# Kernel tuning notes

Hardware: AMD Instinct MI355X
Metric: run time of the kernel (lower is better)

The kernel has to match this reference:

```python
import jax, jax.numpy as jnp
import numpy as np

BATCH, DIM = 32, 512
STDDEV = 0.1


def _annihilation(dim):
    # diag(sqrt(1..dim-1), k=1), complex64
    d = jnp.sqrt(jnp.arange(1, dim, dtype=jnp.float32)).astype(jnp.complex64)
    return jnp.diag(d, k=1)


def setup_inputs() -> dict:
    key = jax.random.key(0)
    ks = jax.random.split(key, 8)
    f = lambda k, shape: jax.random.normal(k, shape, dtype=jnp.float32)
    return {
        'inputs_re': f(ks[0], (BATCH, DIM, DIM)),
        'inputs_im': f(ks[1], (BATCH, DIM, DIM)),
        'theta_1': f(ks[2], (1,)) * STDDEV,
        'theta_2': f(ks[3], (1,)) * STDDEV,
        'r': f(ks[4], (1,)) * STDDEV,
        'bx': f(ks[5], (1,)) * STDDEV,
        'bp': f(ks[6], (1,)) * STDDEV,
        'kappa': f(ks[7], (1,)) * STDDEV,
    }


def _forward(inputs_re, inputs_im, theta_1, theta_2, r, bx, bp, kappa):
    dim = inputs_re.shape[-1]
    x = jax.lax.complex(inputs_re, inputs_im)  # [B, dim, dim] complex64

    a = _annihilation(dim)                     # [dim, dim]
    a_dag = a.conj().T
    n_diag = jnp.arange(dim, dtype=jnp.float32).astype(jnp.complex64)  # number-operator diagonal

    # Rotation operators: expm(-1i*theta*N) with N diagonal -> closed-form diagonal exp (same math)
    th1 = theta_1[0].astype(jnp.complex64)
    th2 = theta_2[0].astype(jnp.complex64)
    R1 = jnp.diag(jnp.exp(-1j * th1 * n_diag))
    R2 = jnp.diag(jnp.exp(-1j * th2 * n_diag))

    # Kerr operator: expm(1i*kappa * (N*N elementwise)) ; N diagonal so N*N = diag(k^2)
    kap = kappa[0].astype(jnp.complex64)
    K = jnp.diag(jnp.exp(1j * kap * n_diag * n_diag))

    # Squeezing: in the TF source, '*' is ELEMENTWISE, and adjoint(a) (subdiag) elementwise
    # times a (superdiag) is the zero matrix -> generator is identically 0 -> S = expm(0) = I.
    # We keep the (zero) generator in the graph so r stays a (zero-grad) primal.
    r_c = r[0].astype(jnp.complex64)
    M_S = 0.5 * (r_c * (a_dag * a) - jnp.conj(r_c) * (a * a_dag))  # exactly zeros
    S = jnp.eye(dim, dtype=jnp.complex64) + M_S

    # Displacement: D = expm(alpha*a_dag - conj(alpha)*a). Generator M is skew-Hermitian,
    # so M = iH with H = -iM Hermitian; D = V diag(exp(i*w)) V^H via eigh (exact, differentiable).
    alpha = jax.lax.complex(bx[0], bp[0])
    M = alpha * a_dag - jnp.conj(alpha) * a
    H = (-1j) * M
    w, V = jnp.linalg.eigh(H)  # w real [dim], V [dim, dim]
    D = (V * jnp.exp(1j * w.astype(jnp.complex64))[None, :]) @ V.conj().T

    # Apply gates in the original order; operators are per-sample identical so
    # broadcast one [dim,dim] matrix over the batch instead of tiling.
    y = jnp.einsum('ij,bjk->bik', R1, x)
    y = jnp.einsum('ij,bjk->bik', S, y)
    y = jnp.einsum('ij,bjk->bik', R2, y)
    y = jnp.einsum('ij,bjk->bik', D, y)
    y = jnp.einsum('ij,bjk->bik', K, y)
    return y


def reference(inputs_re, inputs_im, theta_1, theta_2, r, bx, bp, kappa):
    return _forward(inputs_re, inputs_im, theta_1, theta_2, r, bx, bp, kappa)
```

## Files before the change

kernel.cpp:

```cpp
#include <hip/hip_runtime.h>
#include <hip/hip_fp16.h>

#define DIM 512
#define BATCH 32

typedef _Float16 half8 __attribute__((ext_vector_type(8)));
typedef float floatx4 __attribute__((ext_vector_type(4)));

static __device__ __forceinline__ unsigned short f2h(float f) {
    __half h = __float2half(f);
    return *reinterpret_cast<unsigned short*>(&h);
}

__global__ __launch_bounds__(256) void taylor_tables(const float* __restrict__ bxp,
                                                     const float* __restrict__ bpp,
                                                     const float* __restrict__ th1p,
                                                     const float* __restrict__ th2p,
                                                     const float* __restrict__ kapp,
                                                     float2* __restrict__ E,
                                                     float2* __restrict__ pm,
                                                     float2* __restrict__ pj) {
    if (blockIdx.x == 128) {
        for (int u = threadIdx.x; u < 2 * DIM; u += 256) {
            if (u < DIM) {
                float s, c;
                sincosf(kapp[0] * (float)(u * u), &s, &c);
                pm[u] = make_float2(c, s);
            } else {
                const int j = u - DIM;
                float s, c;
                sincosf(-(th1p[0] + th2p[0]) * (float)j, &s, &c);
                pj[j] = make_float2(c, s);
            }
        }
        return;
    }

    const int wave = (blockIdx.x * blockDim.x + threadIdx.x) >> 6;
    const int lane = threadIdx.x & 63;
    if (wave >= DIM) return;
    const int i = wave;
    const float bx = bxp[0], bp = bpp[0];
    const float invs = 0.5f;
    const int o = lane - 31;
    const int j = i + o;
    const bool jvalid = (j >= 0 && j < DIM);

    float pre = 0.f, pim = 0.f;
    if (o == -1 && i >= 1)      { float g = sqrtf((float)i)       * invs; pre =  bx * g; pim = bp * g; }
    if (o ==  1 && i + 1 < DIM) { float g = sqrtf((float)(i + 1)) * invs; pre = -bx * g; pim = bp * g; }
    float ere = (o == 0 ? 1.f : 0.f) + pre;
    float eim = pim;

    const float gs = (jvalid && j >= 1)       ? sqrtf((float)j)       * invs : 0.f;
    const float hs = (jvalid && j + 1 < DIM)  ? sqrtf((float)(j + 1)) * invs : 0.f;
    const float csup_re = -bx * gs, csup_im = bp * gs;
    const float csub_re =  bx * hs, csub_im = bp * hs;

    for (int k = 2; k <= 30; ++k) {
        const float invk = 1.f / (float)k;
        float pmre = __shfl_up(pre, 1, 64),   pmim = __shfl_up(pim, 1, 64);
        float ppre = __shfl_down(pre, 1, 64), ppim = __shfl_down(pim, 1, 64);
        if (lane == 0)  { pmre = 0.f; pmim = 0.f; }
        if (lane == 63) { ppre = 0.f; ppim = 0.f; }
        float nre = pmre * csup_re - pmim * csup_im + ppre * csub_re - ppim * csub_im;
        float nim = pmre * csup_im + pmim * csup_re + ppre * csub_im + ppim * csub_re;
        pre = nre * invk; pim = nim * invk;
        ere += pre; eim += pim;
    }

    for (int base = 0; base < DIM; base += 64) {
        const int c = base + lane;
        const int src = c - i + 31;
        const float tre = __shfl(ere, src & 63, 64);
        const float tim = __shfl(eim, src & 63, 64);
        float vre = 0.f, vim = 0.f;
        if (src >= 0 && src < 64) { vre = tre; vim = tim; }
        E[i * DIM + c] = make_float2(vre, vim);
    }
}

__global__ __launch_bounds__(256) void csq_fold32(const float2* __restrict__ A,
                                                  unsigned short* __restrict__ Gp,
                                                  const float2* __restrict__ pm,
                                                  const float2* __restrict__ pj) {
    __shared__ float2 At[16][33];
    __shared__ float2 Bt[16][33];
    const int j0 = blockIdx.x * 32, i0 = blockIdx.y * 32;
    const int tid = threadIdx.x;
    const int tx = tid & 15, ty = tid >> 4;
    const int lmin = max(0, max(i0, j0) - 32);
    const int lmax = min(DIM, min(i0, j0) + 64);

    float cre[2][2] = {{0.f}}, cim[2][2] = {{0.f}};
    for (int lt = lmin; lt < lmax; lt += 16) {
        for (int idx = tid; idx < 512; idx += 256) {
            const int r = idx >> 4, c = idx & 15;
            const int l = lt + c;
            At[c][r] = (l < lmax) ? A[(i0 + r) * DIM + l]       : make_float2(0.f, 0.f);
            Bt[c][r] = (l < lmax) ? A[(size_t)l * DIM + j0 + r] : make_float2(0.f, 0.f);
        }
        __syncthreads();
#pragma unroll
        for (int ll = 0; ll < 16; ++ll) {
            float2 a0 = At[ll][ty * 2], a1 = At[ll][ty * 2 + 1];
            float2 b0 = Bt[ll][tx * 2], b1 = Bt[ll][tx * 2 + 1];
            cre[0][0] += a0.x * b0.x - a0.y * b0.y;  cim[0][0] += a0.x * b0.y + a0.y * b0.x;
            cre[0][1] += a0.x * b1.x - a0.y * b1.y;  cim[0][1] += a0.x * b1.y + a0.y * b1.x;
            cre[1][0] += a1.x * b0.x - a1.y * b0.y;  cim[1][0] += a1.x * b0.y + a1.y * b0.x;
            cre[1][1] += a1.x * b1.x - a1.y * b1.y;  cim[1][1] += a1.x * b1.y + a1.y * b1.x;
        }
        __syncthreads();
    }

#pragma unroll
    for (int q = 0; q < 2; ++q) {
        const int m = i0 + ty * 2 + q;
        const float2 km = pm[m];
#pragma unroll
        for (int r = 0; r < 2; ++r) {
            const int j = j0 + tx * 2 + r;
            const float2 tj = pj[j];
            const float r1 = cre[q][r] * tj.x - cim[q][r] * tj.y;
            const float i1 = cre[q][r] * tj.y + cim[q][r] * tj.x;
            const float r2 = r1 * km.x - i1 * km.y;
            const float i2 = r1 * km.y + i1 * km.x;
            *reinterpret_cast<ushort2*>(Gp + (size_t)m * 1024 + 2 * j) =
                make_ushort2(f2h(r2), f2h(-i2));
        }
    }
}

#define XS_STRIDE 72
__global__ __launch_bounds__(256) void apply_fused(const unsigned short* __restrict__ Gp,
                                                   const float* __restrict__ xre,
                                                   const float* __restrict__ xim,
                                                   float* __restrict__ out) {
    __shared__ unsigned short Xs[128 * XS_STRIDE];

    const int k0 = blockIdx.x * 128, m0 = blockIdx.y * 128, b = blockIdx.z;
    const int tid = threadIdx.x, lane = tid & 63, w = tid >> 6;
    const int wr = w >> 1, wc = w & 1;
    const int lr = lane & 15, lk8 = (lane >> 4) * 8;

    const int jmin = max(0, m0 - 64);
    const int jmax = min(DIM, m0 + 192);
    const int nchunk = (jmax - jmin) >> 5;

    const int s_jl = tid & 31;
    const int s_k  = (tid >> 5) << 4;

    const unsigned short* gp = Gp + (size_t)(m0 + wr * 64 + lr) * 1024 + 2 * jmin + lk8;
    const unsigned short* bbase = &Xs[(wc * 64 + lr) * XS_STRIDE + lk8];

    floatx4 acc[4][4];
#pragma unroll
    for (int ms = 0; ms < 4; ++ms)
#pragma unroll
        for (int ns = 0; ns < 4; ++ns) {
            acc[ms][ns][0] = 0.f; acc[ms][ns][1] = 0.f;
            acc[ms][ns][2] = 0.f; acc[ms][ns][3] = 0.f;
        }

    for (int ch = 0; ch < nchunk; ++ch) {
        const size_t xrow = ((size_t)b * DIM + jmin + ch * 32 + s_jl) * DIM + k0 + s_k;
        float4 xr[4], xi[4];
#pragma unroll
        for (int t = 0; t < 4; ++t) xr[t] = *reinterpret_cast<const float4*>(xre + xrow + 4 * t);
#pragma unroll
        for (int t = 0; t < 4; ++t) xi[t] = *reinterpret_cast<const float4*>(xim + xrow + 4 * t);

        __syncthreads();

#pragma unroll
        for (int t = 0; t < 4; ++t) {
            const int kb = s_k + 4 * t;
            *reinterpret_cast<ushort2*>(&Xs[(kb + 0) * XS_STRIDE + 2 * s_jl]) = make_ushort2(f2h(xr[t].x), f2h(xi[t].x));
            *reinterpret_cast<ushort2*>(&Xs[(kb + 1) * XS_STRIDE + 2 * s_jl]) = make_ushort2(f2h(xr[t].y), f2h(xi[t].y));
            *reinterpret_cast<ushort2*>(&Xs[(kb + 2) * XS_STRIDE + 2 * s_jl]) = make_ushort2(f2h(xr[t].z), f2h(xi[t].z));
            *reinterpret_cast<ushort2*>(&Xs[(kb + 3) * XS_STRIDE + 2 * s_jl]) = make_ushort2(f2h(xr[t].w), f2h(xi[t].w));
        }
        __syncthreads();

#pragma unroll
        for (int s = 0; s < 2; ++s) {
            half8 a[4], bb[4];
#pragma unroll
            for (int ms = 0; ms < 4; ++ms)
                a[ms] = *reinterpret_cast<const half8*>(gp + (size_t)ms * 16 * 1024 + ch * 64 + s * 32);
#pragma unroll
            for (int ns = 0; ns < 4; ++ns)
                bb[ns] = *reinterpret_cast<const half8*>(bbase + ns * 16 * XS_STRIDE + s * 32);
#pragma unroll
            for (int ms = 0; ms < 4; ++ms)
#pragma unroll
                for (int ns = 0; ns < 4; ++ns)
                    acc[ms][ns] = __builtin_amdgcn_mfma_f32_16x16x32_f16(a[ms], bb[ns], acc[ms][ns], 0, 0, 0);
        }
    }

    const int crow = (lane >> 4) * 4;
#pragma unroll
    for (int ms = 0; ms < 4; ++ms) {
#pragma unroll
        for (int ns = 0; ns < 4; ++ns) {
            const int kk = k0 + wc * 64 + ns * 16 + lr;
#pragma unroll
            for (int e = 0; e < 4; ++e) {
                const int m = m0 + wr * 64 + ms * 16 + crow + e;
                out[((size_t)b * DIM + m) * DIM + kk] = acc[ms][ns][e];
            }
        }
    }
}

extern "C" void kernel_launch(void* const* d_in, const int* in_sizes, int n_in,
                              void* d_out, int out_size, void* d_ws, size_t ws_size,
                              hipStream_t stream) {
    const float* xre = (const float*)d_in[0];
    const float* xim = (const float*)d_in[1];
    const float* th1 = (const float*)d_in[2];
    const float* th2 = (const float*)d_in[3];
    const float* bx  = (const float*)d_in[5];
    const float* bp  = (const float*)d_in[6];
    const float* kap = (const float*)d_in[7];
    float* out = (float*)d_out;

    char* ws = (char*)d_ws;
    float2* E           = (float2*)ws;
    unsigned short* Gp  = (unsigned short*)(ws + 2u * 1024 * 1024);
    float2* pm          = (float2*)(ws + 3u * 1024 * 1024);
    float2* pj          = pm + DIM;

    hipLaunchKernelGGL(taylor_tables, dim3(129), dim3(256), 0, stream,
                       bx, bp, th1, th2, kap, E, pm, pj);
    hipLaunchKernelGGL(csq_fold32, dim3(16, 16), dim3(256), 0, stream,
                       E, Gp, pm, pj);
    hipLaunchKernelGGL(apply_fused, dim3(4, 4, BATCH), dim3(256), 0, stream,
                       Gp, xre, xim, out);
}
```

Measured before the change: 57.16 us.

## Halve N-tile, double-buffer X staging in LDS, raise occupancy of apply kernel

Shrinks the apply kernel's column tile from 128 to 64, doubling the grid to 1024 blocks. Adds a two-stage LDS ping-pong so the next chunk of X is loaded from global memory while MFMAs run on the current one, with one barrier per chunk instead of two. Sets launch bounds to request 4 blocks per CU. The cost is that each G row tile is re-read by twice as many blocks, and each wave does fewer MFMAs per A-fragment load.

New measurement: 71.46 us. +25.0%, slower.

```diff
diff --git a/kernel.cpp b/kernel.cpp
--- a/kernel.cpp
+++ b/kernel.cpp
@@ -132,13 +132,13 @@
 }
 
 #define XS_STRIDE 72
-__global__ __launch_bounds__(256) void apply_fused(const unsigned short* __restrict__ Gp,
-                                                   const float* __restrict__ xre,
-                                                   const float* __restrict__ xim,
-                                                   float* __restrict__ out) {
-    __shared__ unsigned short Xs[128 * XS_STRIDE];
-
-    const int k0 = blockIdx.x * 128, m0 = blockIdx.y * 128, b = blockIdx.z;
+__global__ __launch_bounds__(256, 4) void apply_fused(const unsigned short* __restrict__ Gp,
+                                                      const float* __restrict__ xre,
+                                                      const float* __restrict__ xim,
+                                                      float* __restrict__ out) {
+    __shared__ unsigned short Xs[2][64 * XS_STRIDE];
+
+    const int k0 = blockIdx.x * 64, m0 = blockIdx.y * 128, b = blockIdx.z;
     const int tid = threadIdx.x, lane = tid & 63, w = tid >> 6;
     const int wr = w >> 1, wc = w & 1;
     const int lr = lane & 15, lk8 = (lane >> 4) * 8;
@@ -148,63 +148,87 @@
     const int nchunk = (jmax - jmin) >> 5;
 
     const int s_jl = tid & 31;
-    const int s_k  = (tid >> 5) << 4;
+    const int s_k  = (tid >> 5) << 3;
 
     const unsigned short* gp = Gp + (size_t)(m0 + wr * 64 + lr) * 1024 + 2 * jmin + lk8;
-    const unsigned short* bbase = &Xs[(wc * 64 + lr) * XS_STRIDE + lk8];
-
-    floatx4 acc[4][4];
+    const size_t xrow0 = ((size_t)b * DIM + jmin + s_jl) * DIM + k0 + s_k;
+
+    floatx4 acc[4][2];
 #pragma unroll
     for (int ms = 0; ms < 4; ++ms)
 #pragma unroll
-        for (int ns = 0; ns < 4; ++ns) {
+        for (int ns = 0; ns < 2; ++ns) {
             acc[ms][ns][0] = 0.f; acc[ms][ns][1] = 0.f;
             acc[ms][ns][2] = 0.f; acc[ms][ns][3] = 0.f;
         }
 
+    float4 xr[2], xi[2];
+#pragma unroll
+    for (int t = 0; t < 2; ++t) {
+        xr[t] = *reinterpret_cast<const float4*>(xre + xrow0 + 4 * t);
+        xi[t] = *reinterpret_cast<const float4*>(xim + xrow0 + 4 * t);
+    }
+#pragma unroll
+    for (int t = 0; t < 2; ++t) {
+        const int kb = s_k + 4 * t;
+        *reinterpret_cast<ushort2*>(&Xs[0][(kb + 0) * XS_STRIDE + 2 * s_jl]) = make_ushort2(f2h(xr[t].x), f2h(xi[t].x));
+        *reinterpret_cast<ushort2*>(&Xs[0][(kb + 1) * XS_STRIDE + 2 * s_jl]) = make_ushort2(f2h(xr[t].y), f2h(xi[t].y));
+        *reinterpret_cast<ushort2*>(&Xs[0][(kb + 2) * XS_STRIDE + 2 * s_jl]) = make_ushort2(f2h(xr[t].z), f2h(xi[t].z));
+        *reinterpret_cast<ushort2*>(&Xs[0][(kb + 3) * XS_STRIDE + 2 * s_jl]) = make_ushort2(f2h(xr[t].w), f2h(xi[t].w));
+    }
+    __syncthreads();
+
+    int cur = 0;
     for (int ch = 0; ch < nchunk; ++ch) {
-        const size_t xrow = ((size_t)b * DIM + jmin + ch * 32 + s_jl) * DIM + k0 + s_k;
-        float4 xr[4], xi[4];
-#pragma unroll
-        for (int t = 0; t < 4; ++t) xr[t] = *reinterpret_cast<const float4*>(xre + xrow + 4 * t);
-#pragma unroll
-        for (int t = 0; t < 4; ++t) xi[t] = *reinterpret_cast<const float4*>(xim + xrow + 4 * t);
-
-        __syncthreads();
-
-#pragma unroll
-        for (int t = 0; t < 4; ++t) {
-            const int kb = s_k + 4 * t;
-            *reinterpret_cast<ushort2*>(&Xs[(kb + 0) * XS_STRIDE + 2 * s_jl]) = make_ushort2(f2h(xr[t].x), f2h(xi[t].x));
-            *reinterpret_cast<ushort2*>(&Xs[(kb + 1) * XS_STRIDE + 2 * s_jl]) = make_ushort2(f2h(xr[t].y), f2h(xi[t].y));
-            *reinterpret_cast<ushort2*>(&Xs[(kb + 2) * XS_STRIDE + 2 * s_jl]) = make_ushort2(f2h(xr[t].z), f2h(xi[t].z));
-            *reinterpret_cast<ushort2*>(&Xs[(kb + 3) * XS_STRIDE + 2 * s_jl]) = make_ushort2(f2h(xr[t].w), f2h(xi[t].w));
-        }
-        __syncthreads();
-
+        const bool has_next = (ch + 1 < nchunk);
+
+        if (has_next) {
+            const size_t xrow = xrow0 + (size_t)(ch + 1) * 32 * DIM;
+#pragma unroll
+            for (int t = 0; t < 2; ++t) {
+                xr[t] = *reinterpret_cast<const float4*>(xre + xrow + 4 * t);
+                xi[t] = *reinterpret_cast<const float4*>(xim + xrow + 4 * t);
+            }
+        }
+
+        const unsigned short* bbase = &Xs[cur][(wc * 32 + lr) * XS_STRIDE + lk8];
 #pragma unroll
         for (int s = 0; s < 2; ++s) {
-            half8 a[4], bb[4];
+            half8 a[4], bb[2];
 #pragma unroll
             for (int ms = 0; ms < 4; ++ms)
                 a[ms] = *reinterpret_cast<const half8*>(gp + (size_t)ms * 16 * 1024 + ch * 64 + s * 32);
 #pragma unroll
-            for (int ns = 0; ns < 4; ++ns)
+            for (int ns = 0; ns < 2; ++ns)
                 bb[ns] = *reinterpret_cast<const half8*>(bbase + ns * 16 * XS_STRIDE + s * 32);
 #pragma unroll
             for (int ms = 0; ms < 4; ++ms)
 #pragma unroll
-                for (int ns = 0; ns < 4; ++ns)
+                for (int ns = 0; ns < 2; ++ns)
                     acc[ms][ns] = __builtin_amdgcn_mfma_f32_16x16x32_f16(a[ms], bb[ns], acc[ms][ns], 0, 0, 0);
         }
+
+        if (has_next) {
+            unsigned short* xdst = Xs[cur ^ 1];
+#pragma unroll
+            for (int t = 0; t < 2; ++t) {
+                const int kb = s_k + 4 * t;
+                *reinterpret_cast<ushort2*>(&xdst[(kb + 0) * XS_STRIDE + 2 * s_jl]) = make_ushort2(f2h(xr[t].x), f2h(xi[t].x));
+                *reinterpret_cast<ushort2*>(&xdst[(kb + 1) * XS_STRIDE + 2 * s_jl]) = make_ushort2(f2h(xr[t].y), f2h(xi[t].y));
+                *reinterpret_cast<ushort2*>(&xdst[(kb + 2) * XS_STRIDE + 2 * s_jl]) = make_ushort2(f2h(xr[t].z), f2h(xi[t].z));
+                *reinterpret_cast<ushort2*>(&xdst[(kb + 3) * XS_STRIDE + 2 * s_jl]) = make_ushort2(f2h(xr[t].w), f2h(xi[t].w));
+            }
+        }
+        __syncthreads();
+        cur ^= 1;
     }
 
     const int crow = (lane >> 4) * 4;
 #pragma unroll
     for (int ms = 0; ms < 4; ++ms) {
 #pragma unroll
-        for (int ns = 0; ns < 4; ++ns) {
-            const int kk = k0 + wc * 64 + ns * 16 + lr;
+        for (int ns = 0; ns < 2; ++ns) {
+            const int kk = k0 + wc * 32 + ns * 16 + lr;
 #pragma unroll
             for (int e = 0; e < 4; ++e) {
                 const int m = m0 + wr * 64 + ms * 16 + crow + e;
@@ -236,6 +260,6 @@
                        bx, bp, th1, th2, kap, E, pm, pj);
     hipLaunchKernelGGL(csq_fold32, dim3(16, 16), dim3(256), 0, stream,
                        E, Gp, pm, pj);
-    hipLaunchKernelGGL(apply_fused, dim3(4, 4, BATCH), dim3(256), 0, stream,
+    hipLaunchKernelGGL(apply_fused, dim3(8, 4, BATCH), dim3(256), 0, stream,
                        Gp, xre, xim, out);
 }
```

## Double-buffer X tiles in LDS with register prefetch and XCD-aware block remap

Applied to the files above, without the earlier changes.

The apply kernel now keeps two LDS buffers for the packed fp16 X tiles and prefetches the next chunks into registers while the MFMA loop runs on the current buffer. This cuts one barrier per chunk and hides global load latency. The grid is flattened and remapped so blocks of the same batch land on the same XCD for better L2 sharing of the operator matrix. It also adds s_setprio around the MFMA sections and launch_bounds(256,2). The cost is more registers (two prefetch sets) and double the LDS per block, which may reduce occupancy. nchunk is even for every tile, so the paired loop stays correct.

After: 60.05 us. 5.1% more time.

```diff
diff --git a/kernel.cpp b/kernel.cpp
--- a/kernel.cpp
+++ b/kernel.cpp
@@ -132,13 +132,20 @@
 }
 
 #define XS_STRIDE 72
-__global__ __launch_bounds__(256) void apply_fused(const unsigned short* __restrict__ Gp,
-                                                   const float* __restrict__ xre,
-                                                   const float* __restrict__ xim,
-                                                   float* __restrict__ out) {
-    __shared__ unsigned short Xs[128 * XS_STRIDE];
-
-    const int k0 = blockIdx.x * 128, m0 = blockIdx.y * 128, b = blockIdx.z;
+__global__ __launch_bounds__(256, 2) void apply_fused(const unsigned short* __restrict__ Gp,
+                                                      const float* __restrict__ xre,
+                                                      const float* __restrict__ xim,
+                                                      float* __restrict__ out) {
+    __shared__ unsigned short Xs[2][128 * XS_STRIDE];
+
+    const int orig = blockIdx.x;
+    const int xcd = orig & 7;
+    const int wgid = xcd * 64 + (orig >> 3);
+    const int b  = wgid >> 4;
+    const int mk = wgid & 15;
+    const int m0 = (mk >> 2) * 128;
+    const int k0 = (mk & 3) * 128;
+
     const int tid = threadIdx.x, lane = tid & 63, w = tid >> 6;
     const int wr = w >> 1, wc = w & 1;
     const int lr = lane & 15, lk8 = (lane >> 4) * 8;
@@ -151,7 +158,7 @@
     const int s_k  = (tid >> 5) << 4;
 
     const unsigned short* gp = Gp + (size_t)(m0 + wr * 64 + lr) * 1024 + 2 * jmin + lk8;
-    const unsigned short* bbase = &Xs[(wc * 64 + lr) * XS_STRIDE + lk8];
+    const size_t xrow0 = ((size_t)b * DIM + jmin + s_jl) * DIM + k0 + s_k;
 
     floatx4 acc[4][4];
 #pragma unroll
@@ -162,41 +169,66 @@
             acc[ms][ns][2] = 0.f; acc[ms][ns][3] = 0.f;
         }
 
-    for (int ch = 0; ch < nchunk; ++ch) {
-        const size_t xrow = ((size_t)b * DIM + jmin + ch * 32 + s_jl) * DIM + k0 + s_k;
-        float4 xr[4], xi[4];
-#pragma unroll
-        for (int t = 0; t < 4; ++t) xr[t] = *reinterpret_cast<const float4*>(xre + xrow + 4 * t);
-#pragma unroll
-        for (int t = 0; t < 4; ++t) xi[t] = *reinterpret_cast<const float4*>(xim + xrow + 4 * t);
-
-        __syncthreads();
-
-#pragma unroll
-        for (int t = 0; t < 4; ++t) {
-            const int kb = s_k + 4 * t;
-            *reinterpret_cast<ushort2*>(&Xs[(kb + 0) * XS_STRIDE + 2 * s_jl]) = make_ushort2(f2h(xr[t].x), f2h(xi[t].x));
-            *reinterpret_cast<ushort2*>(&Xs[(kb + 1) * XS_STRIDE + 2 * s_jl]) = make_ushort2(f2h(xr[t].y), f2h(xi[t].y));
-            *reinterpret_cast<ushort2*>(&Xs[(kb + 2) * XS_STRIDE + 2 * s_jl]) = make_ushort2(f2h(xr[t].z), f2h(xi[t].z));
-            *reinterpret_cast<ushort2*>(&Xs[(kb + 3) * XS_STRIDE + 2 * s_jl]) = make_ushort2(f2h(xr[t].w), f2h(xi[t].w));
-        }
-        __syncthreads();
-
-#pragma unroll
-        for (int s = 0; s < 2; ++s) {
-            half8 a[4], bb[4];
-#pragma unroll
-            for (int ms = 0; ms < 4; ++ms)
-                a[ms] = *reinterpret_cast<const half8*>(gp + (size_t)ms * 16 * 1024 + ch * 64 + s * 32);
-#pragma unroll
-            for (int ns = 0; ns < 4; ++ns)
-                bb[ns] = *reinterpret_cast<const half8*>(bbase + ns * 16 * XS_STRIDE + s * 32);
-#pragma unroll
-            for (int ms = 0; ms < 4; ++ms)
-#pragma unroll
-                for (int ns = 0; ns < 4; ++ns)
-                    acc[ms][ns] = __builtin_amdgcn_mfma_f32_16x16x32_f16(a[ms], bb[ns], acc[ms][ns], 0, 0, 0);
-        }
+    float4 Axr[4], Axi[4], Bxr[4], Bxi[4];
+
+#define LOADX(XR, XI, CH)                                                        \
+    {                                                                            \
+        const size_t xrow = xrow0 + (size_t)(CH) * 32 * DIM;                     \
+        _Pragma("unroll")                                                        \
+        for (int t = 0; t < 4; ++t) {                                            \
+            XR[t] = *reinterpret_cast<const float4*>(xre + xrow + 4 * t);        \
+            XI[t] = *reinterpret_cast<const float4*>(xim + xrow + 4 * t);        \
+        }                                                                        \
+    }
+
+#define PACK(XR, XI, BUF)                                                        \
+    {                                                                            \
+        _Pragma("unroll")                                                        \
+        for (int t = 0; t < 4; ++t) {                                            \
+            const int kb = s_k + 4 * t;                                          \
+            *reinterpret_cast<ushort2*>(&Xs[BUF][(kb + 0) * XS_STRIDE + 2 * s_jl]) = make_ushort2(f2h(XR[t].x), f2h(XI[t].x)); \
+            *reinterpret_cast<ushort2*>(&Xs[BUF][(kb + 1) * XS_STRIDE + 2 * s_jl]) = make_ushort2(f2h(XR[t].y), f2h(XI[t].y)); \
+            *reinterpret_cast<ushort2*>(&Xs[BUF][(kb + 2) * XS_STRIDE + 2 * s_jl]) = make_ushort2(f2h(XR[t].z), f2h(XI[t].z)); \
+            *reinterpret_cast<ushort2*>(&Xs[BUF][(kb + 3) * XS_STRIDE + 2 * s_jl]) = make_ushort2(f2h(XR[t].w), f2h(XI[t].w)); \
+        }                                                                        \
+    }
+
+#define MFMA_CHUNK(BUF, CH)                                                      \
+    {                                                                            \
+        const unsigned short* bbase = &Xs[BUF][(wc * 64 + lr) * XS_STRIDE + lk8];\
+        __builtin_amdgcn_s_setprio(1);                                           \
+        _Pragma("unroll")                                                        \
+        for (int s = 0; s < 2; ++s) {                                            \
+            half8 a[4], bb[4];                                                   \
+            _Pragma("unroll")                                                    \
+            for (int ms = 0; ms < 4; ++ms)                                       \
+                a[ms] = *reinterpret_cast<const half8*>(gp + (size_t)ms * 16 * 1024 + (CH) * 64 + s * 32); \
+            _Pragma("unroll")                                                    \
+            for (int ns = 0; ns < 4; ++ns)                                       \
+                bb[ns] = *reinterpret_cast<const half8*>(bbase + ns * 16 * XS_STRIDE + s * 32); \
+            _Pragma("unroll")                                                    \
+            for (int ms = 0; ms < 4; ++ms)                                       \
+                _Pragma("unroll")                                                \
+                for (int ns = 0; ns < 4; ++ns)                                   \
+                    acc[ms][ns] = __builtin_amdgcn_mfma_f32_16x16x32_f16(a[ms], bb[ns], acc[ms][ns], 0, 0, 0); \
+        }                                                                        \
+        __builtin_amdgcn_s_setprio(0);                                           \
+    }
+
+    LOADX(Axr, Axi, 0);
+    LOADX(Bxr, Bxi, 1);
+    PACK(Axr, Axi, 0);
+    __syncthreads();
+
+    for (int ch = 0; ch < nchunk; ch += 2) {
+        if (ch + 2 < nchunk) LOADX(Axr, Axi, ch + 2);
+        MFMA_CHUNK(0, ch);
+        PACK(Bxr, Bxi, 1);
+        __syncthreads();
+        if (ch + 3 < nchunk) LOADX(Bxr, Bxi, ch + 3);
+        MFMA_CHUNK(1, ch + 1);
+        if (ch + 2 < nchunk) PACK(Axr, Axi, 0);
+        __syncthreads();
     }
 
     const int crow = (lane >> 4) * 4;
@@ -212,6 +244,9 @@
             }
         }
     }
+#undef LOADX
+#undef PACK
+#undef MFMA_CHUNK
 }
 
 extern "C" void kernel_launch(void* const* d_in, const int* in_sizes, int n_in,
@@ -236,6 +271,6 @@
                        bx, bp, th1, th2, kap, E, pm, pj);
     hipLaunchKernelGGL(csq_fold32, dim3(16, 16), dim3(256), 0, stream,
                        E, Gp, pm, pj);
-    hipLaunchKernelGGL(apply_fused, dim3(4, 4, BATCH), dim3(256), 0, stream,
+    hipLaunchKernelGGL(apply_fused, dim3(512), dim3(256), 0, stream,
                        Gp, xre, xim, out);
 }
```
